# Performance work log

Measured on AMD Instinct MI355X. Metric: run time of the kernel, lower is better.

Reference implementation:

```python
import jax, jax.numpy as jnp
import numpy as np

VOCAB = 100000
E = 256      # embedding dim == projection dim (required by layer-axis concat)
H = 2048     # lstm hidden dim
P = 256      # projection dim
B, T = 8, 96
CELL_CLIP = 3.0
PROJ_CLIP = 3.0
NUM_LAYERS = 2


def setup_inputs() -> dict:
    key = jax.random.key(0)
    ks = jax.random.split(key, 8)
    tokens = jax.random.randint(ks[0], (B, T), 0, VOCAB, dtype=jnp.int32)
    mask = jnp.ones((B, T, 1), dtype=jnp.float32)
    embed_table = jax.random.normal(ks[1], (VOCAB + 1, E), dtype=jnp.float32) * 0.05
    # stacked LSTM weights: index 0=fwd L0, 1=fwd L1, 2=bwd L0, 3=bwd L1
    Wk = jax.random.normal(ks[2], (4, E, 4 * H), dtype=jnp.float32) * 0.02
    Wr = jax.random.normal(ks[3], (4, P, 4 * H), dtype=jnp.float32) * 0.02
    b = jnp.zeros((4, 4 * H), dtype=jnp.float32)
    Wp = jax.random.normal(ks[4], (4, H, P), dtype=jnp.float32) * 0.02
    elmo_w = jnp.zeros((NUM_LAYERS + 1,), dtype=jnp.float32)
    gamma = jnp.ones((1,), dtype=jnp.float32)
    return {"tokens": tokens, "mask": mask, "embed_table": embed_table,
            "Wk": Wk, "Wr": Wr, "b": b, "Wp": Wp,
            "elmo_w": elmo_w, "gamma": gamma}


def _lstm_proj(x, m, Wk, Wr, b, Wp, reverse):
    # x: [B,T,E], m: [B,T,1]. LSTM with cell clip, output projection, proj clip.
    if reverse:
        x = jnp.flip(x, 1)
        m = jnp.flip(m, 1)
    xs = jnp.swapaxes(x, 0, 1)                     # [T,B,E]
    ms = jnp.swapaxes(m, 0, 1)                     # [T,B,1]
    xW = jnp.einsum('tbe,ef->tbf', xs, Wk) + b     # precompute input gates [T,B,4H]

    def step(carry, inp):
        h, c = carry                               # h:[B,P], c:[B,H]
        zx, mt = inp
        z = zx + h @ Wr                            # [B,4H]
        i, f, g, o = jnp.split(z, 4, axis=-1)
        i = jax.nn.sigmoid(i)
        f = jax.nn.sigmoid(f)
        g = jnp.tanh(g)
        o = jax.nn.sigmoid(o)
        c_new = jnp.clip(f * c + i * g, -CELL_CLIP, CELL_CLIP)
        h_new = jnp.clip((o * jnp.tanh(c_new)) @ Wp, -PROJ_CLIP, PROJ_CLIP)
        keep = mt > 0
        h_new = jnp.where(keep, h_new, h)
        c_new = jnp.where(keep, c_new, c)
        return (h_new, c_new), h_new

    h0 = jnp.zeros((x.shape[0], Wp.shape[1]), x.dtype)
    c0 = jnp.zeros((x.shape[0], Wp.shape[0]), x.dtype)
    _, hs = jax.lax.scan(step, (h0, c0), (xW, ms))
    out = jnp.swapaxes(hs, 0, 1)                   # [B,T,P]
    if reverse:
        out = jnp.flip(out, 1)
    return out


def _elmo_layers(tokens, mask, embed_table, Wk, Wr, b, Wp):
    emb = embed_table[tokens]                      # [B,T,E]
    dir_outs = []
    for rev, base in ((False, 0), (True, 2)):
        inp = emb
        outs = []
        for l in range(NUM_LAYERS):
            out = _lstm_proj(inp, mask, Wk[base + l], Wr[base + l],
                             b[base + l], Wp[base + l], rev)
            inp = inp + out if l > 0 else out      # skip connection on layer > 0
            outs.append(inp)
        dir_outs.append(outs)
    fwd, bwd = dir_outs
    layers = [jnp.concatenate([emb, emb], -1)]
    layers += [jnp.concatenate([f, bb], -1) for f, bb in zip(fwd, bwd)]
    return jnp.stack(layers, axis=1)               # [B, L+1, T, 2P]


def reference(tokens, mask, embed_table, Wk, Wr, b, Wp, elmo_w, gamma):
    all_emb = _elmo_layers(tokens, mask, embed_table, Wk, Wr, b, Wp)
    m = mask[:, None, :, :]                        # [B,1,T,1]
    num = jnp.sum(mask, axis=(1, 2))[:, None]      # [B,1]
    xm = all_emb * m
    mean = jnp.sum(xm, axis=(2, 3)) / num          # [B,L+1]
    mean = mean[:, :, None, None]
    var = jnp.sum(((xm - mean) * m) ** 2, axis=(2, 3)) / num
    var = var[:, :, None, None]
    normed = (all_emb - mean) / jnp.sqrt(var + 1e-12)
    w = jax.nn.softmax(elmo_w)[None, :, None, None]
    weighted = jnp.sum(w * normed, axis=1) * gamma  # [B,T,2P]
    return weighted
```

## Files before the change

### kernel.cpp

```cpp
#include <hip/hip_runtime.h>
#include <hip/hip_bf16.h>

#define DEVFN __device__ __forceinline__

static constexpr size_t OFF_CTRS   = 0;
static constexpr size_t OFF_STATS  = 131328;
static constexpr size_t OFF_EW     = 131584;
static constexpr size_t OFF_MASK32 = 131840;
static constexpr size_t OFF_EMB    = 135168;
static constexpr size_t OFF_WPT    = 921600;
static constexpr size_t OFF_BIAS   = 9310208;
static constexpr size_t OFF_XW     = 9441280;
static constexpr size_t OFF_OUT0   = 59772928;
static constexpr size_t OFF_OUT1   = 61345792;
static constexpr size_t OFF_Y      = 62918656;
static constexpr size_t OFF_H      = 75501568;

template<int BF>
DEVFN float ldin(const void* p, size_t i) {
  if (BF) {
    unsigned short u = ((const unsigned short*)p)[i];
    return __uint_as_float(((unsigned)u) << 16);
  }
  return ((const float*)p)[i];
}
DEVFN float ldraw(const void* p, size_t i, int bf) {
  if (bf) {
    unsigned short u = ((const unsigned short*)p)[i];
    return __uint_as_float(((unsigned)u) << 16);
  }
  return ((const float*)p)[i];
}

DEVFN float sigm(float x) { return 1.f / (1.f + __expf(-x)); }
DEVFN float clip3(float x) { return fminf(fmaxf(x, -3.f), 3.f); }

DEVFN int detect_bf(const void* maskp) {
  return (((const unsigned*)maskp)[0] == 0x3F800000u) ? 0 : 1;
}

template<int BF>
__global__ void prep_k(const int* __restrict__ tokens, const void* __restrict__ maskp,
                       const void* __restrict__ et, const void* __restrict__ bias,
                       const void* __restrict__ ew, const void* __restrict__ gm,
                       const void* __restrict__ Wp,
                       float* bias32, float* mask32, float* ew32, float* emb, float* WpT) {
  if (detect_bf(maskp) != BF) return;
  const int bid = blockIdx.x, tid = threadIdx.x;

  if (bid < 132) {
    size_t i = (size_t)bid * 256 + tid;
    if (i >= 33540) return;
    if (i < 32768)       bias32[i] = ldin<BF>(bias, i);
    else if (i < 33536)  mask32[i - 32768] = ldin<BF>(maskp, i - 32768);
    else if (i < 33539)  ew32[i - 33536]   = ldin<BF>(ew, i - 33536);
    else                 ew32[3] = ldin<BF>(gm, 0);
    return;
  }

  if (bid < 644) {
    const int r = bid - 132;
    const int kt = r & 31, pt = (r >> 5) & 3, dl = r >> 7;
    __shared__ float tile[64][65];
    for (int it = 0; it < 4; ++it) {
      int lin = it * 1024 + tid * 4;
      int kk = lin >> 6, pp = lin & 63;
      size_t src = ((size_t)(dl * 2048 + kt * 64 + kk)) * 256 + pt * 64 + pp;
      float v0, v1, v2, v3;
      if (BF) {
        const unsigned short* sp = (const unsigned short*)Wp + src;
        v0 = __uint_as_float(((unsigned)sp[0]) << 16);
        v1 = __uint_as_float(((unsigned)sp[1]) << 16);
        v2 = __uint_as_float(((unsigned)sp[2]) << 16);
        v3 = __uint_as_float(((unsigned)sp[3]) << 16);
      } else {
        float4 v = *(const float4*)((const float*)Wp + src);
        v0 = v.x; v1 = v.y; v2 = v.z; v3 = v.w;
      }
      tile[pp + 0][kk] = v0; tile[pp + 1][kk] = v1; tile[pp + 2][kk] = v2; tile[pp + 3][kk] = v3;
    }
    __syncthreads();
    for (int it = 0; it < 4; ++it) {
      int lin = it * 1024 + tid * 4;
      int pr = lin >> 6, kc = lin & 63;
      float4 o;
      o.x = tile[pr][kc + 0]; o.y = tile[pr][kc + 1]; o.z = tile[pr][kc + 2]; o.w = tile[pr][kc + 3];
      *(float4*)(WpT + ((size_t)(dl * 256 + pt * 64 + pr)) * 2048 + kt * 64 + kc) = o;
    }
    return;
  }

  const int bt = bid - 644;
  const int tok = tokens[bt];
  emb[(size_t)bt * 256 + tid] = ldin<BF>(et, (size_t)tok * 256 + tid);
}

template<int BF>
__global__ __launch_bounds__(256) void xw_gemm_k(
    const void* __restrict__ maskp, const float* __restrict__ x_fwd, const float* __restrict__ x_bwd,
    const void* __restrict__ Wk, const float* __restrict__ bias32, float* __restrict__ xW, int layer) {
  if (detect_bf(maskp) != BF) return;
  const int nt = blockIdx.x, mt = blockIdx.y, dir = blockIdx.z;
  const int dl = dir * 2 + layer;
  const float* xb = dir ? x_bwd : x_fwd;
  const int tid = threadIdx.x;

  __shared__ float As[16][68];
  __shared__ float Bs[16][68];

  float acc[4][4] = {};
  const int tx = tid & 15, ty = tid >> 4;

  const int am = tid >> 2;
  const int ak = (tid & 3) * 4;
  const int m_glob = mt * 64 + am;
  const int t_ = m_glob >> 3, b_ = m_glob & 7;
  const int tau = dir ? (95 - t_) : t_;
  const float* arow = xb + ((size_t)(b_ * 96 + tau)) * 256;

  const int bk = tid >> 4, bn = (tid & 15) * 4;

  for (int kb = 0; kb < 256; kb += 16) {
    float4 av = *(const float4*)(arow + kb + ak);
    As[ak + 0][am] = av.x; As[ak + 1][am] = av.y; As[ak + 2][am] = av.z; As[ak + 3][am] = av.w;

    size_t bidx = ((size_t)dl * 256 + (kb + bk)) * 8192 + (size_t)nt * 64 + bn;
    float b0, b1, b2, b3;
    if (BF) {
      ushort4 uv = *(const ushort4*)((const unsigned short*)Wk + bidx);
      b0 = __uint_as_float(((unsigned)uv.x) << 16);
      b1 = __uint_as_float(((unsigned)uv.y) << 16);
      b2 = __uint_as_float(((unsigned)uv.z) << 16);
      b3 = __uint_as_float(((unsigned)uv.w) << 16);
    } else {
      float4 fv = *(const float4*)((const float*)Wk + bidx);
      b0 = fv.x; b1 = fv.y; b2 = fv.z; b3 = fv.w;
    }
    Bs[bk][bn + 0] = b0; Bs[bk][bn + 1] = b1; Bs[bk][bn + 2] = b2; Bs[bk][bn + 3] = b3;
    __syncthreads();

#pragma unroll
    for (int kk = 0; kk < 16; ++kk) {
      float a0 = As[kk][ty * 4 + 0], a1 = As[kk][ty * 4 + 1], a2 = As[kk][ty * 4 + 2], a3 = As[kk][ty * 4 + 3];
      float c0 = Bs[kk][tx * 4 + 0], c1 = Bs[kk][tx * 4 + 1], c2 = Bs[kk][tx * 4 + 2], c3 = Bs[kk][tx * 4 + 3];
      acc[0][0] = fmaf(a0, c0, acc[0][0]); acc[0][1] = fmaf(a0, c1, acc[0][1]);
      acc[0][2] = fmaf(a0, c2, acc[0][2]); acc[0][3] = fmaf(a0, c3, acc[0][3]);
      acc[1][0] = fmaf(a1, c0, acc[1][0]); acc[1][1] = fmaf(a1, c1, acc[1][1]);
      acc[1][2] = fmaf(a1, c2, acc[1][2]); acc[1][3] = fmaf(a1, c3, acc[1][3]);
      acc[2][0] = fmaf(a2, c0, acc[2][0]); acc[2][1] = fmaf(a2, c1, acc[2][1]);
      acc[2][2] = fmaf(a2, c2, acc[2][2]); acc[2][3] = fmaf(a2, c3, acc[2][3]);
      acc[3][0] = fmaf(a3, c0, acc[3][0]); acc[3][1] = fmaf(a3, c1, acc[3][1]);
      acc[3][2] = fmaf(a3, c2, acc[3][2]); acc[3][3] = fmaf(a3, c3, acc[3][3]);
    }
    __syncthreads();
  }

  const int n0 = nt * 64 + tx * 4;
#pragma unroll
  for (int i = 0; i < 4; ++i) {
    int m = mt * 64 + ty * 4 + i;
    int tt = m >> 3, bb = m & 7;
    float4 o;
    o.x = acc[i][0] + bias32[dl * 8192 + n0 + 0];
    o.y = acc[i][1] + bias32[dl * 8192 + n0 + 1];
    o.z = acc[i][2] + bias32[dl * 8192 + n0 + 2];
    o.w = acc[i][3] + bias32[dl * 8192 + n0 + 3];
    *(float4*)(xW + (size_t)((dir * 96 + tt) * 8 + bb) * 8192 + n0) = o;
  }
}

DEVFN void flat_poll(const int* slots, int tid, int ep) {
  const int* a = slots + tid * 16;
  for (;;) {
    int v0 = __hip_atomic_load(a + 0,  __ATOMIC_RELAXED, __HIP_MEMORY_SCOPE_AGENT);
    int v1 = __hip_atomic_load(a + 4,  __ATOMIC_RELAXED, __HIP_MEMORY_SCOPE_AGENT);
    int v2 = __hip_atomic_load(a + 8,  __ATOMIC_RELAXED, __HIP_MEMORY_SCOPE_AGENT);
    int v3 = __hip_atomic_load(a + 12, __ATOMIC_RELAXED, __HIP_MEMORY_SCOPE_AGENT);
    bool ok = (v0 >= ep) & (v1 >= ep) & (v2 >= ep) & (v3 >= ep);
    if (__all(ok)) break;
    __builtin_amdgcn_s_sleep(1);
  }
}

__global__ __launch_bounds__(256, 2) void scan_kernel(
    const float* __restrict__ xW, const void* __restrict__ WrRaw, const void* __restrict__ maskp,
    const float* __restrict__ WpT, const float* __restrict__ mask32,
    float* __restrict__ out, float* __restrict__ hbuf, float* __restrict__ ybuf,
    int* ctrs, int layer) {
  const int tid = threadIdx.x;
  const int w = blockIdx.x;
  const int dir = w >> 8;
  const int g = w & 255;
  const int dl = dir * 2 + layer;

  __shared__ __align__(16) float wr_s[256 * 32];
  __shared__ __align__(16) float h_lds[2048];
  __shared__ float4 wp4_s[512];
  __shared__ float4 zpart[288];
  __shared__ float  z_s[32 * 9];
  __shared__ __align__(16) float xw_s[256];
  __shared__ float  mask_s[768];
  __shared__ float  c_s[64];
  __shared__ float  red_s[8];

  int* slots  = ctrs + (layer * 2 + dir) * 4096;
  int* myslot = slots + g * 4;
  int ep = 0;
  const int bf = detect_bf(maskp);

  {
    const size_t wrbase = (size_t)dl * 256 * 8192;
    for (int i = tid; i < 8192; i += 256) {
      int k = i >> 5, col = i & 31;
      wr_s[i] = ldraw(WrRaw, wrbase + (size_t)k * 8192 + (size_t)(col >> 3) * 2048 + g * 8 + (col & 7), bf);
    }
    const float4* wrow = (const float4*)(WpT + ((size_t)(dl * 256 + g)) * 2048);
    for (int i = tid; i < 512; i += 256) wp4_s[i] = wrow[i];
    for (int i = tid; i < 768; i += 256) mask_s[i] = mask32[i];
  }
  if (tid < 64) c_s[tid] = 0.f;

  const int ks = tid >> 6, colq = (tid >> 3) & 7, lb = tid & 7;
  const float4* wr4 = (const float4*)wr_s;
  const float4* xw4 = (const float4*)xw_s;

  for (int t = 0; t < 96; ++t) {
    const int tau = dir ? (95 - t) : t;
    const float* h_cur = hbuf + ((size_t)(t * 2 + dir)) * 2048;
    float* h_nxt = hbuf + ((size_t)((t + 1) * 2 + dir)) * 2048;
    float* y_t   = ybuf + ((size_t)(t * 2 + dir)) * 16384;

    float xwv;
    {
      int b = tid >> 5, col = tid & 31;
      xwv = xW[(size_t)((dir * 96 + t) * 8 + b) * 8192 + (col >> 3) * 2048 + g * 8 + (col & 7)];
    }

    if (t == 0) {
      ((float4*)h_lds)[tid * 2 + 0] = make_float4(0.f, 0.f, 0.f, 0.f);
      ((float4*)h_lds)[tid * 2 + 1] = make_float4(0.f, 0.f, 0.f, 0.f);
    } else {
      ((float4*)h_lds)[tid * 2 + 0] = ((const float4*)h_cur)[tid * 2 + 0];
      ((float4*)h_lds)[tid * 2 + 1] = ((const float4*)h_cur)[tid * 2 + 1];
    }
    __syncthreads();

    {
      float4 acc = make_float4(0.f, 0.f, 0.f, 0.f);
#pragma unroll 16
      for (int i = 0; i < 64; ++i) {
        int k = (ks << 6) + i;
        float hv = h_lds[k * 8 + lb];
        float4 wv = wr4[k * 8 + colq];
        acc.x = fmaf(hv, wv.x, acc.x); acc.y = fmaf(hv, wv.y, acc.y);
        acc.z = fmaf(hv, wv.z, acc.z); acc.w = fmaf(hv, wv.w, acc.w);
      }
      zpart[(ks * 8 + colq) * 9 + lb] = acc;
      xw_s[tid] = xwv;
    }
    __syncthreads();

    ++ep;
    if (tid < 64) {
      {
        const int b3 = tid & 7, cq = tid >> 3;
        float4 z0 = zpart[(0 * 8 + cq) * 9 + b3];
        float4 z1 = zpart[(1 * 8 + cq) * 9 + b3];
        float4 z2 = zpart[(2 * 8 + cq) * 9 + b3];
        float4 z3 = zpart[(3 * 8 + cq) * 9 + b3];
        float4 xv = xw4[b3 * 8 + cq];
        z_s[(cq * 4 + 0) * 9 + b3] = z0.x + z1.x + z2.x + z3.x + xv.x;
        z_s[(cq * 4 + 1) * 9 + b3] = z0.y + z1.y + z2.y + z3.y + xv.y;
        z_s[(cq * 4 + 2) * 9 + b3] = z0.z + z1.z + z2.z + z3.z + xv.z;
        z_s[(cq * 4 + 3) * 9 + b3] = z0.w + z1.w + z2.w + z3.w + xv.w;
        const int cell = cq;
        float zi = z_s[(0  + cell) * 9 + b3];
        float zf = z_s[(8  + cell) * 9 + b3];
        float zg = z_s[(16 + cell) * 9 + b3];
        float zo = z_s[(24 + cell) * 9 + b3];
        float ig = sigm(zi), fg = sigm(zf), gg = tanhf(zg), og = sigm(zo);
        float cold = c_s[tid];
        float cc = clip3(fg * cold + ig * gg);
        float yv = og * tanhf(cc);
        float m = mask_s[b3 * 96 + tau];
        c_s[tid] = (m > 0.f) ? cc : cold;
        __hip_atomic_store(&y_t[b3 * 2048 + g * 8 + cell], yv, __ATOMIC_RELAXED, __HIP_MEMORY_SCOPE_AGENT);
      }
      asm volatile("s_waitcnt vmcnt(0)" ::: "memory");
      if (tid == 0)
        __hip_atomic_store(myslot, ep, __ATOMIC_RELAXED, __HIP_MEMORY_SCOPE_AGENT);
      flat_poll(slots, tid, ep);
    }
    __syncthreads();

    {
      const int b = tid >> 5, kq = tid & 31;
      const float4* yb = (const float4*)y_t + b * 512;
      float s = 0.f;
#pragma unroll 8
      for (int i = 0; i < 16; ++i) {
        int k4 = i * 32 + kq;
        float4 yv = yb[k4];
        float4 wv = wp4_s[k4];
        s = fmaf(yv.x, wv.x, s); s = fmaf(yv.y, wv.y, s);
        s = fmaf(yv.z, wv.z, s); s = fmaf(yv.w, wv.w, s);
      }
      s += __shfl_down(s, 16, 32);
      s += __shfl_down(s, 8, 32);
      s += __shfl_down(s, 4, 32);
      s += __shfl_down(s, 2, 32);
      s += __shfl_down(s, 1, 32);
      if (kq == 0) red_s[b] = s;
    }
    __syncthreads();

    ++ep;
    if (tid < 64) {
      float hv = 0.f;
      if (tid < 8) {
        float hc = clip3(red_s[tid]);
        float m = mask_s[tid * 96 + tau];
        float hp = h_lds[g * 8 + tid];
        hv = (m > 0.f) ? hc : hp;
        __hip_atomic_store(&h_nxt[g * 8 + tid], hv, __ATOMIC_RELAXED, __HIP_MEMORY_SCOPE_AGENT);
      }
      asm volatile("s_waitcnt vmcnt(0)" ::: "memory");
      if (tid == 0)
        __hip_atomic_store(myslot, ep, __ATOMIC_RELAXED, __HIP_MEMORY_SCOPE_AGENT);
      flat_poll(slots, tid, ep);
      if (tid < 8)
        out[(size_t)((dir * 8 + tid) * 96 + tau) * 256 + g] = hv;
    }
    __syncthreads();
  }
}

DEVFN float layer_val(int l, int b, int t, int f, const float* emb, const float* out0, const float* out1) {
  const int half = f >> 8, p = f & 255;
  if (l == 0) return emb[(size_t)(b * 96 + t) * 256 + p];
  const size_t o = ((size_t)((half * 8 + b) * 96 + t)) * 256 + p;
  float v = out0[o];
  if (l == 2) v += out1[o];
  return v;
}

__global__ void mixA_k(const float* emb, const float* out0, const float* out1,
                       const float* mask32, float* stats) {
  const int b = blockIdx.x / 3, l = blockIdx.x % 3;
  float s1 = 0.f, s2 = 0.f;
  for (int idx = threadIdx.x; idx < 96 * 512; idx += 256) {
    int t = idx >> 9, f = idx & 511;
    float v = layer_val(l, b, t, f, emb, out0, out1);
    float m = mask32[b * 96 + t];
    s1 += m * v; s2 += m * v * v;
  }
  for (int off = 32; off; off >>= 1) { s1 += __shfl_down(s1, off); s2 += __shfl_down(s2, off); }
  __shared__ float p1[4], p2[4];
  if ((threadIdx.x & 63) == 0) { p1[threadIdx.x >> 6] = s1; p2[threadIdx.x >> 6] = s2; }
  __syncthreads();
  if (threadIdx.x == 0) {
    float S1 = p1[0] + p1[1] + p1[2] + p1[3];
    float S2 = p2[0] + p2[1] + p2[2] + p2[3];
    float num = 0.f;
    for (int t = 0; t < 96; ++t) num += mask32[b * 96 + t];
    float mean = S1 / num;
    float var = S2 / num - 2.f * mean * mean + 512.f * mean * mean;
    stats[(b * 3 + l) * 2 + 0] = mean;
    stats[(b * 3 + l) * 2 + 1] = rsqrtf(var + 1e-12f);
  }
}

__global__ void mixB_k(const void* maskp, const float* emb, const float* out0, const float* out1,
                       const float* stats, const float* ew32, void* outp) {
  const int idx = blockIdx.x * 256 + threadIdx.x;
  const int b = idx / 49152;
  const int r = idx % 49152;
  const int t = r >> 9, f = r & 511;
  float w0 = ew32[0], w1 = ew32[1], w2 = ew32[2], gm = ew32[3];
  float mx = fmaxf(w0, fmaxf(w1, w2));
  float e0 = __expf(w0 - mx), e1 = __expf(w1 - mx), e2 = __expf(w2 - mx);
  float inv = 1.f / (e0 + e1 + e2);
  float wl[3] = {e0 * inv, e1 * inv, e2 * inv};
  float acc = 0.f;
#pragma unroll
  for (int l = 0; l < 3; ++l) {
    float v = layer_val(l, b, t, f, emb, out0, out1);
    acc += wl[l] * (v - stats[(b * 3 + l) * 2]) * stats[(b * 3 + l) * 2 + 1];
  }
  acc *= gm;
  if (detect_bf(maskp)) ((__hip_bfloat16*)outp)[idx] = __float2bfloat16(acc);
  else                  ((float*)outp)[idx] = acc;
}

extern "C" void kernel_launch(void* const* d_in, const int* in_sizes, int n_in,
                              void* d_out, int out_size, void* d_ws, size_t ws_size,
                              hipStream_t stream) {
  const int*  tokens = (const int*)d_in[0];
  const void* maskp  = d_in[1];
  const void* embt   = d_in[2];
  const void* Wk     = d_in[3];
  const void* WrRaw  = d_in[4];
  const void* bias   = d_in[5];
  const void* Wp     = d_in[6];
  const void* ew     = d_in[7];
  const void* gm     = d_in[8];

  char* ws = (char*)d_ws;
  int*   ctrs   = (int*)(ws + OFF_CTRS);
  float* stats  = (float*)(ws + OFF_STATS);
  float* ew32   = (float*)(ws + OFF_EW);
  float* mask32 = (float*)(ws + OFF_MASK32);
  float* emb    = (float*)(ws + OFF_EMB);
  float* wpt    = (float*)(ws + OFF_WPT);
  float* bias32 = (float*)(ws + OFF_BIAS);
  float* xW     = (float*)(ws + OFF_XW);
  float* out0   = (float*)(ws + OFF_OUT0);
  float* out1   = (float*)(ws + OFF_OUT1);
  float* ybuf   = (float*)(ws + OFF_Y);
  float* hbuf   = (float*)(ws + OFF_H);

  hipMemsetAsync(d_ws, 0, 131072, stream);

  prep_k<0><<<1412, 256, 0, stream>>>(tokens, maskp, embt, bias, ew, gm, Wp,
                                      bias32, mask32, ew32, emb, wpt);
  prep_k<1><<<1412, 256, 0, stream>>>(tokens, maskp, embt, bias, ew, gm, Wp,
                                      bias32, mask32, ew32, emb, wpt);

  xw_gemm_k<0><<<dim3(128, 12, 2), 256, 0, stream>>>(maskp, emb, emb, Wk, bias32, xW, 0);
  xw_gemm_k<1><<<dim3(128, 12, 2), 256, 0, stream>>>(maskp, emb, emb, Wk, bias32, xW, 0);

  int l0 = 0, l1 = 1;
  {
    void* args[] = {&xW, &WrRaw, &maskp, &wpt, &mask32, &out0, &hbuf, &ybuf, &ctrs, &l0};
    hipError_t e = hipLaunchCooperativeKernel((void*)scan_kernel, dim3(512), dim3(256), args, 0, stream);
    if (e != hipSuccess)
      scan_kernel<<<512, 256, 0, stream>>>(xW, WrRaw, maskp, wpt, mask32, out0, hbuf, ybuf, ctrs, 0);
  }

  float* x_fwd = out0;
  float* x_bwd = out0 + (size_t)8 * 96 * 256;
  xw_gemm_k<0><<<dim3(128, 12, 2), 256, 0, stream>>>(maskp, x_fwd, x_bwd, Wk, bias32, xW, 1);
  xw_gemm_k<1><<<dim3(128, 12, 2), 256, 0, stream>>>(maskp, x_fwd, x_bwd, Wk, bias32, xW, 1);

  {
    void* args[] = {&xW, &WrRaw, &maskp, &wpt, &mask32, &out1, &hbuf, &ybuf, &ctrs, &l1};
    hipError_t e = hipLaunchCooperativeKernel((void*)scan_kernel, dim3(512), dim3(256), args, 0, stream);
    if (e != hipSuccess)
      scan_kernel<<<512, 256, 0, stream>>>(xW, WrRaw, maskp, wpt, mask32, out1, hbuf, ybuf, ctrs, 1);
  }

  mixA_k<<<24, 256, 0, stream>>>(emb, out0, out1, mask32, stats);
  mixB_k<<<1536, 256, 0, stream>>>(maskp, emb, out0, out1, stats, ew32, d_out);
}
```

Baseline: 2.742 ms.

## Replace per-block barrier slots with grouped atomic counters and prefetch next xW

The grid barrier changes from 256 per-block flag slots, each scanned by polling 4 slots per thread, to 64 cache-line counters. Each group of 4 blocks fetch-adds one counter, and each of 64 polling threads reads a single counter against a target of 4*ep. The load of the input-gate term for the next timestep is also moved into the projection phase of the current step, so its latency is hidden instead of exposed at the start of each step. Atomic contention on the shared counters rises slightly, but each poll touches fewer lines.

```diff
diff --git a/kernel.cpp b/kernel.cpp
--- a/kernel.cpp
+++ b/kernel.cpp
@@ -169,18 +169,6 @@
   }
 }
 
-DEVFN void flat_poll(const int* slots, int tid, int ep) {
-  const int* a = slots + tid * 16;
-  for (;;) {
-    int v0 = __hip_atomic_load(a + 0,  __ATOMIC_RELAXED, __HIP_MEMORY_SCOPE_AGENT);
-    int v1 = __hip_atomic_load(a + 4,  __ATOMIC_RELAXED, __HIP_MEMORY_SCOPE_AGENT);
-    int v2 = __hip_atomic_load(a + 8,  __ATOMIC_RELAXED, __HIP_MEMORY_SCOPE_AGENT);
-    int v3 = __hip_atomic_load(a + 12, __ATOMIC_RELAXED, __HIP_MEMORY_SCOPE_AGENT);
-    bool ok = (v0 >= ep) & (v1 >= ep) & (v2 >= ep) & (v3 >= ep);
-    if (__all(ok)) break;
-    __builtin_amdgcn_s_sleep(1);
-  }
-}
 
 __global__ __launch_bounds__(256, 2) void scan_kernel(
     const float* __restrict__ xW, const void* __restrict__ WrRaw, const void* __restrict__ maskp,
@@ -203,8 +191,9 @@
   __shared__ float  c_s[64];
   __shared__ float  red_s[8];
 
-  int* slots  = ctrs + (layer * 2 + dir) * 4096;
-  int* myslot = slots + g * 4;
+  int* base   = ctrs + (layer * 2 + dir) * 4096;
+  int* aline  = base + (g >> 2) * 64;
+  int* myline = base + (tid & 63) * 64;
   int ep = 0;
   const int bf = detect_bf(maskp);
 
@@ -223,18 +212,15 @@
   const int ks = tid >> 6, colq = (tid >> 3) & 7, lb = tid & 7;
   const float4* wr4 = (const float4*)wr_s;
   const float4* xw4 = (const float4*)xw_s;
+  const int pb = tid >> 5, pcol = tid & 31;
+
+  float xwv = xW[(size_t)((dir * 96 + 0) * 8 + pb) * 8192 + (pcol >> 3) * 2048 + g * 8 + (pcol & 7)];
 
   for (int t = 0; t < 96; ++t) {
     const int tau = dir ? (95 - t) : t;
     const float* h_cur = hbuf + ((size_t)(t * 2 + dir)) * 2048;
     float* h_nxt = hbuf + ((size_t)((t + 1) * 2 + dir)) * 2048;
     float* y_t   = ybuf + ((size_t)(t * 2 + dir)) * 16384;
-
-    float xwv;
-    {
-      int b = tid >> 5, col = tid & 31;
-      xwv = xW[(size_t)((dir * 96 + t) * 8 + b) * 8192 + (col >> 3) * 2048 + g * 8 + (col & 7)];
-    }
 
     if (t == 0) {
       ((float4*)h_lds)[tid * 2 + 0] = make_float4(0.f, 0.f, 0.f, 0.f);
@@ -288,8 +274,13 @@
       }
       asm volatile("s_waitcnt vmcnt(0)" ::: "memory");
       if (tid == 0)
-        __hip_atomic_store(myslot, ep, __ATOMIC_RELAXED, __HIP_MEMORY_SCOPE_AGENT);
-      flat_poll(slots, tid, ep);
+        __hip_atomic_fetch_add(aline, 1, __ATOMIC_RELAXED, __HIP_MEMORY_SCOPE_AGENT);
+      const int tgt = 4 * ep;
+      int v = __hip_atomic_load(myline, __ATOMIC_RELAXED, __HIP_MEMORY_SCOPE_AGENT);
+      while (!__all(v >= tgt)) {
+        __builtin_amdgcn_s_sleep(1);
+        v = __hip_atomic_load(myline, __ATOMIC_RELAXED, __HIP_MEMORY_SCOPE_AGENT);
+      }
     }
     __syncthreads();
 
@@ -305,6 +296,8 @@
         s = fmaf(yv.x, wv.x, s); s = fmaf(yv.y, wv.y, s);
         s = fmaf(yv.z, wv.z, s); s = fmaf(yv.w, wv.w, s);
       }
+      if (t < 95)
+        xwv = xW[(size_t)((dir * 96 + (t + 1)) * 8 + pb) * 8192 + (pcol >> 3) * 2048 + g * 8 + (pcol & 7)];
       s += __shfl_down(s, 16, 32);
       s += __shfl_down(s, 8, 32);
       s += __shfl_down(s, 4, 32);
@@ -326,8 +319,13 @@
       }
       asm volatile("s_waitcnt vmcnt(0)" ::: "memory");
       if (tid == 0)
-        __hip_atomic_store(myslot, ep, __ATOMIC_RELAXED, __HIP_MEMORY_SCOPE_AGENT);
-      flat_poll(slots, tid, ep);
+        __hip_atomic_fetch_add(aline, 1, __ATOMIC_RELAXED, __HIP_MEMORY_SCOPE_AGENT);
+      const int tgt = 4 * ep;
+      int v = __hip_atomic_load(myline, __ATOMIC_RELAXED, __HIP_MEMORY_SCOPE_AGENT);
+      while (!__all(v >= tgt)) {
+        __builtin_amdgcn_s_sleep(1);
+        v = __hip_atomic_load(myline, __ATOMIC_RELAXED, __HIP_MEMORY_SCOPE_AGENT);
+      }
       if (tid < 8)
         out[(size_t)((dir * 8 + tid) * 96 + tau) * 256 + g] = hv;
     }
```

Result: faster. 2.425 ms (-11.6%).
